# Optimization experiments

Hardware: AMD Instinct MI355X
Metric: run time of the kernel (lower is better)

## Reference

```python
import jax, jax.numpy as jnp
import numpy as np

B, N, F, U, S = 64, 4096, 2, 16, 2


def setup_inputs() -> dict:
    key = jax.random.key(0)
    ks = jax.random.split(key, 7)
    inputs = jax.random.normal(ks[0], (B, F * N), dtype=jnp.float32)
    state = jax.random.normal(ks[1], (B, U * N), dtype=jnp.float32)

    def random_walk(k):
        a = jax.random.uniform(k, (N, N), dtype=jnp.float32)
        return a / jnp.sum(a, axis=1, keepdims=True)  # row-stochastic like D^-1 A

    support0 = random_walk(ks[2])
    support1 = random_walk(ks[3])
    kshape = ((F + U) * S, U)
    scale = jnp.float32(1.0 / np.sqrt(kshape[0]))
    r_kernel = jax.random.normal(ks[4], kshape, dtype=jnp.float32) * scale
    u_kernel = jax.random.normal(ks[5], kshape, dtype=jnp.float32) * scale
    c_kernel = jax.random.normal(ks[6], kshape, dtype=jnp.float32) * scale
    return {"inputs": inputs, "state": state, "support0": support0,
            "support1": support1, "r_kernel": r_kernel, "u_kernel": u_kernel,
            "c_kernel": c_kernel}


def _diffuse(x, supports):
    # x: (B, C, N); K.dot(x, support.T)[b,c,m] = sum_n x[b,c,n] * support[m,n]
    return jnp.concatenate([jnp.einsum('bcn,mn->bcm', x, s) for s in supports], axis=1)


def reference(inputs, state, support0, support1, r_kernel, u_kernel, c_kernel):
    supports = (support0, support1)
    feats = inputs.reshape(B, F, N)
    prev = state.reshape(B, U, N)

    h = _diffuse(feats, supports).transpose(0, 2, 1)   # (B, N, S*F)
    st = _diffuse(prev, supports).transpose(0, 2, 1)   # (B, N, S*U)
    hs = jnp.concatenate([h, st], axis=-1)             # (B, N, S*(F+U))

    r = jax.nn.sigmoid(hs @ r_kernel)                  # (B, N, U)
    u = jax.nn.sigmoid(hs @ u_kernel)                  # (B, N, U)

    prev_t = prev.transpose(0, 2, 1)                   # (B, N, U)
    r_prev = (r * prev_t).transpose(0, 2, 1)           # (B, U, N)
    c_state = _diffuse(r_prev, supports).transpose(0, 2, 1)  # (B, N, S*U)
    c = jnp.tanh(jnp.concatenate([h, c_state], axis=-1) @ c_kernel)  # (B, N, U)

    z = u * prev_t + (1.0 - u) * c                     # (B, N, U)
    # original: activation=None -> linear, then K.reshape(output, (-1, units*num_nodes))
    return z.reshape(B, U * N)
```

## Files before the change

kernel.cpp:

```cpp
#include <hip/hip_runtime.h>
#include <cstdint>

#define KDIM 4096
#define NNODE 4096
#define KSPLIT 2
#define TSTEPS 128
#define THALF (TSTEPS / KSPLIT)

typedef __bf16 bf16x8 __attribute__((ext_vector_type(8)));
typedef float floatx4 __attribute__((ext_vector_type(4)));

__device__ __forceinline__ uint16_t f2b(float f) {
  union { float f; uint32_t u; } v; v.f = f;
  uint32_t u = v.u;
  return (uint16_t)((u + 0x7FFFu + ((u >> 16) & 1u)) >> 16);
}
__device__ __forceinline__ float b2f(uint16_t h) {
  union { uint32_t u; float f; } v; v.u = ((uint32_t)h) << 16; return v.f;
}
__device__ __forceinline__ uint32_t pack2(float a, float b) {
  return (uint32_t)f2b(a) | ((uint32_t)f2b(b) << 16);
}


__global__ __launch_bounds__(256) void cvt_supports(
    const float* __restrict__ s0, const float* __restrict__ s1,
    uint16_t* __restrict__ d0, uint16_t* __restrict__ d1) {
  const float* src = blockIdx.z ? s1 : s0;
  uint16_t* dst = blockIdx.z ? d1 : d0;
  const int c16 = blockIdx.x, kb = blockIdx.y;
  const int col_in = threadIdx.x >> 4, k8 = threadIdx.x & 15;
  const int col = c16 * 16 + col_in;
  const int k = kb * 128 + k8 * 8;
  const float* p = src + (size_t)col * KDIM + k;
  float4 v0 = *(const float4*)p;
  float4 v1 = *(const float4*)(p + 4);
  uint4 o;
  o.x = pack2(v0.x, v0.y); o.y = pack2(v0.z, v0.w);
  o.z = pack2(v1.x, v1.y); o.w = pack2(v1.z, v1.w);
  size_t off = ((size_t)(c16 * 128 + kb * 4 + (k8 >> 2))) * 512 +
               (size_t)((k8 & 3) * 16 + col_in) * 8;
  *(uint4*)(dst + off) = o;
}

__global__ __launch_bounds__(256) void pack_x1(
    const float* __restrict__ inp, const float* __restrict__ st,
    uint16_t* __restrict__ X1) {
  const int r16 = blockIdx.x, kb = blockIdx.y;
  const int row_in = threadIdx.x >> 4, k8 = threadIdx.x & 15;
  const int row = r16 * 16 + row_in;
  const int k = kb * 128 + k8 * 8;
  int b = row / 18, c = row - b * 18;
  const float* p = (c < 2) ? (inp + (size_t)b * 8192 + (size_t)c * 4096 + k)
                           : (st + (size_t)b * 65536 + (size_t)(c - 2) * 4096 + k);
  float4 v0 = *(const float4*)p;
  float4 v1 = *(const float4*)(p + 4);
  uint4 o;
  o.x = pack2(v0.x, v0.y); o.y = pack2(v0.z, v0.w);
  o.z = pack2(v1.x, v1.y); o.w = pack2(v1.z, v1.w);
  size_t off = ((size_t)(r16 * 128 + kb * 4 + (k8 >> 2))) * 512 +
               (size_t)((k8 & 3) * 16 + row_in) * 8;
  *(uint4*)(X1 + off) = o;
}

__device__ __forceinline__ void gl_lds16(const uint16_t* g, uint16_t* l) {
  __builtin_amdgcn_global_load_lds(
      (const __attribute__((address_space(1))) uint32_t*)g,
      (__attribute__((address_space(3))) uint32_t*)l, 16, 0, 0);
}

template <int MODE>
__global__ __launch_bounds__(256) void gemm_frag(
    const uint16_t* __restrict__ Af, const uint16_t* __restrict__ S0f,
    const uint16_t* __restrict__ S1f, uint16_t* __restrict__ D) {
  constexpr int CPB = (MODE == 1) ? 18 : 16;
  constexpr int OUTC = (MODE == 1) ? 36 : 32;
  constexpr size_t PSTRIDE = (size_t)64 * OUTC * NNODE;
  constexpr int NCH = THALF;

  __shared__ uint16_t sAB[4][16][512];

  const int lane = threadIdx.x & 63, wave = threadIdx.x >> 6;
  const int wr = wave >> 1, wc = wave & 1;
  const int s = blockIdx.z & 1, ks = blockIdx.z >> 1;
  const uint16_t* __restrict__ Bf = s ? S1f : S0f;
  const int yF = blockIdx.y * 8;
  const int xF = blockIdx.x * 8;
  const int tBeg = ks * THALF;

  const bool isB = wave >= 2;
  const int fbase = (wave & 1) * 4;
  const uint16_t* Gw = (isB ? Bf : Af) +
      ((size_t)((isB ? xF : yF) + fbase) * 128 + (size_t)tBeg) * 512 +
      (size_t)lane * 8;
  const int slotw = (isB ? 8 : 0) + fbase;

  floatx4 acc[4][4];
#pragma unroll
  for (int i = 0; i < 4; ++i)
#pragma unroll
    for (int j = 0; j < 4; ++j) acc[i][j] = (floatx4){0.f, 0.f, 0.f, 0.f};

  auto STAGE = [&](int bi, int c) {
    const uint16_t* gt = Gw + (size_t)c * 512;
#pragma unroll
    for (int i = 0; i < 4; ++i)
      gl_lds16(gt + (size_t)i * 65536, &sAB[bi][slotw + i][0]);
  };

  STAGE(0, 0);
  STAGE(1, 1);

  for (int c = 0; c < NCH; ++c) {
    int cl = c + 2; if (cl > NCH - 1) cl = NCH - 1;
    STAGE((c + 2) & 3, cl);
    asm volatile("s_waitcnt vmcnt(8)" ::: "memory");
    __builtin_amdgcn_sched_barrier(0);
    __builtin_amdgcn_s_barrier();
    __builtin_amdgcn_sched_barrier(0);
    const int bi = c & 3;
    bf16x8 a[4], b[4];
#pragma unroll
    for (int rt = 0; rt < 4; ++rt)
      a[rt] = *(const bf16x8*)&sAB[bi][wr * 4 + rt][lane * 8];
#pragma unroll
    for (int ct = 0; ct < 4; ++ct)
      b[ct] = *(const bf16x8*)&sAB[bi][8 + wc * 4 + ct][lane * 8];
    __builtin_amdgcn_s_setprio(1);
#pragma unroll
    for (int rt = 0; rt < 4; ++rt)
#pragma unroll
      for (int ct = 0; ct < 4; ++ct)
        acc[rt][ct] = __builtin_amdgcn_mfma_f32_16x16x32_bf16(
            a[rt], b[ct], acc[rt][ct], 0, 0, 0);
    __builtin_amdgcn_s_setprio(0);
    __builtin_amdgcn_sched_barrier(0);
  }

  uint16_t* Dp = D + (size_t)ks * PSTRIDE;
#pragma unroll
  for (int rt = 0; rt < 4; ++rt) {
#pragma unroll
    for (int r = 0; r < 4; ++r) {
      int rowg = yF * 16 + wr * 64 + rt * 16 + (lane >> 4) * 4 + r;
      int b = rowg / CPB, c = rowg - b * CPB;
      int jj;
      if (MODE == 1) jj = (c < 2) ? (2 * s + c) : (4 + 16 * s + (c - 2));
      else jj = 16 * s + c;
      uint16_t* drow = Dp + (size_t)(b * OUTC + jj) * NNODE;
#pragma unroll
      for (int ct = 0; ct < 4; ++ct) {
        int colg = xF * 16 + wc * 64 + ct * 16 + (lane & 15);
        drow[colg] = f2b(acc[rt][ct][r]);
      }
    }
  }
}

__global__ __launch_bounds__(256) void stage2(
    const uint16_t* __restrict__ P1, const float* __restrict__ state,
    const float* __restrict__ rk, const float* __restrict__ uk,
    uint16_t* __restrict__ X2f, float* __restrict__ U) {
  constexpr size_t PS = (size_t)64 * 36 * NNODE;
  __shared__ float s_rk[576], s_uk[576];
  __shared__ uint16_t s_x2[16 * 264];
  for (int i = threadIdx.x; i < 576; i += 256) { s_rk[i] = rk[i]; s_uk[i] = uk[i]; }
  __syncthreads();
  const int b = blockIdx.x >> 4, nb = blockIdx.x & 15;
  const int i = threadIdx.x;
  const int n = nb * 256 + i;
  float hs[36];
  const uint16_t* p = P1 + (size_t)b * 36 * NNODE + n;
#pragma unroll
  for (int j = 0; j < 36; ++j)
    hs[j] = b2f(p[(size_t)j * NNODE]) + b2f(p[PS + (size_t)j * NNODE]);
  float ar[16], au[16];
#pragma unroll
  for (int k = 0; k < 16; ++k) { ar[k] = 0.f; au[k] = 0.f; }
#pragma unroll
  for (int j = 0; j < 36; ++j) {
    float h = hs[j];
#pragma unroll
    for (int k = 0; k < 16; ++k) {
      ar[k] += h * s_rk[j * 16 + k];
      au[k] += h * s_uk[j * 16 + k];
    }
  }
  const float* sp = state + (size_t)b * 65536 + n;
#pragma unroll
  for (int k = 0; k < 16; ++k) {
    float r = 1.f / (1.f + __expf(-ar[k]));
    float uu = 1.f / (1.f + __expf(-au[k]));
    float prev = sp[(size_t)k * NNODE];
    s_x2[k * 264 + i] = f2b(r * prev);
    U[(size_t)(b * 16 + k) * NNODE + n] = uu;
  }
  __syncthreads();
  uint16_t* region = X2f + ((size_t)b * 128 + nb * 8) * 512;
#pragma unroll
  for (int rr = 0; rr < 2; ++rr) {
    int fid = rr * 256 + i;
    int kk = fid & 15, qq = (fid >> 4) & 3, tl = fid >> 6;
    uint4 v = *(const uint4*)&s_x2[kk * 264 + tl * 32 + qq * 8];
    *(uint4*)(region + (size_t)fid * 8) = v;
  }
}

__global__ __launch_bounds__(256) void stage4(
    const uint16_t* __restrict__ P1, const uint16_t* __restrict__ P3,
    const float* __restrict__ U, const float* __restrict__ state,
    const float* __restrict__ ck, float* __restrict__ out) {
  constexpr size_t PS1 = (size_t)64 * 36 * NNODE;
  constexpr size_t PS3 = (size_t)64 * 32 * NNODE;
  __shared__ float s_ck[576];
  for (int i = threadIdx.x; i < 576; i += 256) s_ck[i] = ck[i];
  __syncthreads();
  int idx = blockIdx.x * 256 + threadIdx.x;
  int b = idx >> 12, n = idx & 4095;
  float hv[36];
  const uint16_t* p1 = P1 + (size_t)b * 36 * NNODE + n;
#pragma unroll
  for (int j = 0; j < 4; ++j)
    hv[j] = b2f(p1[(size_t)j * NNODE]) + b2f(p1[PS1 + (size_t)j * NNODE]);
  const uint16_t* p3 = P3 + (size_t)b * 32 * NNODE + n;
#pragma unroll
  for (int j = 0; j < 32; ++j)
    hv[4 + j] = b2f(p3[(size_t)j * NNODE]) + b2f(p3[PS3 + (size_t)j * NNODE]);
  float ac[16];
#pragma unroll
  for (int k = 0; k < 16; ++k) ac[k] = 0.f;
#pragma unroll
  for (int j = 0; j < 36; ++j) {
    float h = hv[j];
#pragma unroll
    for (int k = 0; k < 16; ++k) ac[k] += h * s_ck[j * 16 + k];
  }
  const float* sp = state + (size_t)b * 65536 + n;
  const float* up = U + (size_t)b * 16 * NNODE + n;
  float z[16];
#pragma unroll
  for (int k = 0; k < 16; ++k) {
    float e = __expf(2.f * ac[k]);
    float c = 1.f - 2.f / (e + 1.f);
    float uu = up[(size_t)k * NNODE];
    float prev = sp[(size_t)k * NNODE];
    z[k] = uu * prev + (1.f - uu) * c;
  }
  float4* po = (float4*)(out + (size_t)b * 65536 + (size_t)n * 16);
#pragma unroll
  for (int k4 = 0; k4 < 4; ++k4)
    po[k4] = make_float4(z[k4 * 4], z[k4 * 4 + 1], z[k4 * 4 + 2], z[k4 * 4 + 3]);
}

extern "C" void kernel_launch(void* const* d_in, const int* in_sizes, int n_in,
                              void* d_out, int out_size, void* d_ws, size_t ws_size,
                              hipStream_t stream) {
  const float* inputs = (const float*)d_in[0];
  const float* state = (const float*)d_in[1];
  const float* s0 = (const float*)d_in[2];
  const float* s1 = (const float*)d_in[3];
  const float* rk = (const float*)d_in[4];
  const float* uk = (const float*)d_in[5];
  const float* ck = (const float*)d_in[6];
  float* out = (float*)d_out;
  char* ws = (char*)d_ws;

  uint16_t* S0f = (uint16_t*)(ws);
  uint16_t* S1f = (uint16_t*)(ws + 33554432);
  uint16_t* X1f = (uint16_t*)(ws + 67108864);
  uint16_t* X2f = (uint16_t*)(ws + 67108864);
  uint16_t* P1 = (uint16_t*)(ws + 76546048);
  float* U = (float*)(ws + 114294784);
  uint16_t* P3 = (uint16_t*)(ws + 131072000);

  cvt_supports<<<dim3(256, 32, 2), 256, 0, stream>>>(s0, s1, S0f, S1f);
  pack_x1<<<dim3(72, 32), 256, 0, stream>>>(inputs, state, X1f);
  gemm_frag<1><<<dim3(32, 9, 2 * KSPLIT), 256, 0, stream>>>(X1f, S0f, S1f, P1);
  stage2<<<1024, 256, 0, stream>>>(P1, state, rk, uk, X2f, U);
  gemm_frag<3><<<dim3(32, 8, 2 * KSPLIT), 256, 0, stream>>>(X2f, S0f, S1f, P3);
  stage4<<<1024, 256, 0, stream>>>(P1, P3, U, state, ck, out);
}
```

Measured before the change: 365.4 us.

## Deepen GEMM prefetch to three stages and double-buffer LDS-to-register fragments

Restructures the main GEMM loop so global-to-LDS staging runs three chunks ahead instead of two. LDS fragments for the next chunk are loaded into a second register set while MFMAs run on the current one, with an lgkmcnt wait so the reads overlap the math. Adds launch_bounds occupancy hint of 2 blocks. The cost is roughly double the fragment registers and a 4x unrolled loop, which could raise register pressure or cause spills, and the deeper prefetch relies on the 4-slot LDS ring being safe from overwrites.

```diff
diff --git a/kernel.cpp b/kernel.cpp
--- a/kernel.cpp
+++ b/kernel.cpp
@@ -70,7 +70,7 @@
 }
 
 template <int MODE>
-__global__ __launch_bounds__(256) void gemm_frag(
+__global__ __launch_bounds__(256, 2) void gemm_frag(
     const uint16_t* __restrict__ Af, const uint16_t* __restrict__ S0f,
     const uint16_t* __restrict__ S1f, uint16_t* __restrict__ D) {
   constexpr int CPB = (MODE == 1) ? 18 : 16;
@@ -108,24 +108,16 @@
       gl_lds16(gt + (size_t)i * 65536, &sAB[bi][slotw + i][0]);
   };
 
-  STAGE(0, 0);
-  STAGE(1, 1);
-
-  for (int c = 0; c < NCH; ++c) {
-    int cl = c + 2; if (cl > NCH - 1) cl = NCH - 1;
-    STAGE((c + 2) & 3, cl);
-    asm volatile("s_waitcnt vmcnt(8)" ::: "memory");
-    __builtin_amdgcn_sched_barrier(0);
-    __builtin_amdgcn_s_barrier();
-    __builtin_amdgcn_sched_barrier(0);
-    const int bi = c & 3;
-    bf16x8 a[4], b[4];
+  auto LDREG = [&](int bi, bf16x8* a, bf16x8* b) {
 #pragma unroll
     for (int rt = 0; rt < 4; ++rt)
       a[rt] = *(const bf16x8*)&sAB[bi][wr * 4 + rt][lane * 8];
 #pragma unroll
     for (int ct = 0; ct < 4; ++ct)
       b[ct] = *(const bf16x8*)&sAB[bi][8 + wc * 4 + ct][lane * 8];
+  };
+
+  auto MFMA16 = [&](bf16x8* a, bf16x8* b) {
     __builtin_amdgcn_s_setprio(1);
 #pragma unroll
     for (int rt = 0; rt < 4; ++rt)
@@ -134,8 +126,42 @@
         acc[rt][ct] = __builtin_amdgcn_mfma_f32_16x16x32_bf16(
             a[rt], b[ct], acc[rt][ct], 0, 0, 0);
     __builtin_amdgcn_s_setprio(0);
-    __builtin_amdgcn_sched_barrier(0);
-  }
+  };
+
+  STAGE(0, 0);
+  STAGE(1, 1);
+  STAGE(2, 2);
+  asm volatile("s_waitcnt vmcnt(8)" ::: "memory");
+  __builtin_amdgcn_sched_barrier(0);
+  __builtin_amdgcn_s_barrier();
+  __builtin_amdgcn_sched_barrier(0);
+  bf16x8 aA[4], bA[4], aB[4], bB[4];
+  LDREG(0, aA, bA);
+
+#define GEMM_ITER(J, RDBUF, STBUF, CURA, CURB, NXTA, NXTB)                  \
+  {                                                                         \
+    int cl = c0 + 3 + (J);                                                  \
+    if (cl > NCH - 1) cl = NCH - 1;       \
+    STAGE((STBUF), cl);                                                     \
+    asm volatile("s_waitcnt vmcnt(8)" ::: "memory");                        \
+    __builtin_amdgcn_sched_barrier(0);                                      \
+    __builtin_amdgcn_s_barrier();                                           \
+    __builtin_amdgcn_sched_barrier(0);                                      \
+    LDREG((RDBUF), NXTA, NXTB);                                             \
+    asm volatile("s_waitcnt lgkmcnt(8)" ::: "memory");                      \
+    __builtin_amdgcn_sched_barrier(0);                                      \
+    MFMA16(CURA, CURB);                                                     \
+    __builtin_amdgcn_sched_barrier(0);                                      \
+  }
+
+  for (int m = 0; m < NCH / 4; ++m) {
+    const int c0 = m * 4;
+    GEMM_ITER(0, 1, 3, aA, bA, aB, bB)
+    GEMM_ITER(1, 2, 0, aB, bB, aA, bA)
+    GEMM_ITER(2, 3, 1, aA, bA, aB, bB)
+    GEMM_ITER(3, 0, 2, aB, bB, aA, bA)
+  }
+#undef GEMM_ITER
 
   uint16_t* Dp = D + (size_t)ks * PSTRIDE;
 #pragma unroll
```

Result: faster. 352.5 us (-3.5%).
